# Performance work log

Measured on AMD Instinct MI355X. Metric: run time of the kernel, lower is better.

Reference implementation:

```python
import jax, jax.numpy as jnp
import numpy as np

FIELD_DIMS = [100000] * 39
EMBED_DIM = 16
BATCH = 4096
BETA = 0.01
EPS = 1e-4
OFFSETS = np.concatenate([[0], np.cumsum(FIELD_DIMS)[:-1]]).astype(np.int32)


def setup_inputs() -> dict:
    key = jax.random.key(0)
    k1, k2 = jax.random.split(key)
    x = jax.random.randint(k1, (BATCH, len(FIELD_DIMS)), 0, 100000, dtype=jnp.int32)
    emb_table = jax.random.normal(k2, (sum(FIELD_DIMS), EMBED_DIM), dtype=jnp.float32) * 0.01
    return {"x": x, "emb_table": emb_table}


def reference(x, emb_table):
    # x: [B, F] per-field indices; add per-field offsets then gather -> [B, F, d]
    idx = x + jnp.asarray(OFFSETS)[None, :]
    x_emb = emb_table[idx]
    B, F, _ = x_emb.shape

    # ---- alignment loss: mean over all i<j pairs and fields of ||x_i[f]-x_j[f]||^2.
    # Exact Gram identity: sum_{i<j} ||xi-xj||^2 = B*sum_i ||xi||^2 - ||sum_i xi||^2 (per field).
    sq = jnp.sum(x_emb * x_emb, axis=-1)          # [B, F]
    s = jnp.sum(x_emb, axis=0)                     # [F, d]
    pair_sum = B * jnp.sum(sq) - jnp.sum(s * s)
    n_pairs = B * (B - 1) // 2
    align_loss = pair_sum / (n_pairs * F)

    # ---- uniformity loss: mean of cosine-like similarity over all field pairs per sample.
    frac = jnp.einsum('bfd,bgd->bfg', x_emb, x_emb)   # [B, F, F]
    norms = jnp.sqrt(sq)                               # [B, F]
    denom = norms[:, :, None] * norms[:, None, :] + EPS
    uniform_loss = jnp.mean(frac / denom)

    return (align_loss + uniform_loss) * BETA
```

## Files before the change

kernel.cpp:

```cpp
#include <hip/hip_runtime.h>


#define BATCH   4096
#define NF      39
#define ED      16
#define SPB     8
#define THREADS 256
#define NPAIRS  (NF * (NF + 1) / 2)
#define ROWF    (NF * ED)
#define EPS     1e-4f
#define BETA    0.01

__global__ __launch_bounds__(THREADS) void cl4ctr_main(
    const int* __restrict__ x, const float* __restrict__ emb,
    float* __restrict__ s_glob,
    float* __restrict__ scal)
{
    __shared__ __align__(16) float e[SPB][ROWF];
    __shared__ float norms[SPB][NF + 1];
    __shared__ int   sidx[SPB * NF];
    __shared__ float wred[2][4];

    const int tid = threadIdx.x;
    const int b0  = blockIdx.x * SPB;

    for (int t = tid; t < SPB * NF; t += THREADS)
        sidx[t] = x[b0 * NF + t];
    __syncthreads();

    for (int p = tid; p < SPB * NF * 4; p += THREADS) {
        int si = p / (NF * 4);
        int r  = p - si * (NF * 4);
        int f  = r >> 2, q = r & 3;
        size_t row = (size_t)sidx[si * NF + f] + (size_t)f * 100000u;
        float4 v = *(const float4*)(emb + row * ED + q * 4);
        *(float4*)&e[si][f * ED + q * 4] = v;
    }
    __syncthreads();

    for (int t = tid; t < ROWF; t += THREADS) {
        float a = 0.f;
#pragma unroll
        for (int si = 0; si < SPB; ++si) a += e[si][t];
        atomicAdd(&s_glob[t], a);
    }

    float sq_local = 0.f;
    for (int t = tid; t < SPB * NF; t += THREADS) {
        int si = t / NF, f = t - si * NF;
        const float4* r4 = (const float4*)&e[si][f * ED];
        float4 a = r4[0], b = r4[1], c = r4[2], d = r4[3];
        float sq = a.x*a.x + a.y*a.y + a.z*a.z + a.w*a.w
                 + b.x*b.x + b.y*b.y + b.z*b.z + b.w*b.w
                 + c.x*c.x + c.y*c.y + c.z*c.z + c.w*c.w
                 + d.x*d.x + d.y*d.y + d.z*d.z + d.w*d.w;
        norms[si][f] = sqrtf(sq);
        sq_local += sq;
    }
    __syncthreads();

    float uni = 0.f;
    for (int p = tid; p < SPB * NPAIRS; p += THREADS) {
        int si = p / NPAIRS;
        int k  = p - si * NPAIRS;
        int f = (int)((79.0f - sqrtf((float)(6241 - 8 * k))) * 0.5f);
        if (f > NF - 1) f = NF - 1;
        while (f * (79 - f) / 2 > k) --f;
        while ((f + 1) * (78 - f) / 2 <= k) ++f;
        int g = f + (k - f * (79 - f) / 2);

        const float4* rf = (const float4*)&e[si][f * ED];
        const float4* rg = (const float4*)&e[si][g * ED];
        float4 a0 = rf[0], a1 = rf[1], a2 = rf[2], a3 = rf[3];
        float4 b0 = rg[0], b1 = rg[1], b2 = rg[2], b3 = rg[3];
        float dot = a0.x*b0.x + a0.y*b0.y + a0.z*b0.z + a0.w*b0.w
                  + a1.x*b1.x + a1.y*b1.y + a1.z*b1.z + a1.w*b1.w
                  + a2.x*b2.x + a2.y*b2.y + a2.z*b2.z + a2.w*b2.w
                  + a3.x*b3.x + a3.y*b3.y + a3.z*b3.z + a3.w*b3.w;
        float w = (f == g) ? 1.f : 2.f;
        uni += w * dot / (norms[si][f] * norms[si][g] + EPS);
    }

#pragma unroll
    for (int off = 32; off > 0; off >>= 1) {
        uni      += __shfl_down(uni, off, 64);
        sq_local += __shfl_down(sq_local, off, 64);
    }
    int lane = tid & 63, wv = tid >> 6;
    if (lane == 0) { wred[0][wv] = uni; wred[1][wv] = sq_local; }
    __syncthreads();
    if (tid == 0) {
        atomicAdd(&scal[0], wred[0][0] + wred[0][1] + wred[0][2] + wred[0][3]);
        atomicAdd(&scal[1], wred[1][0] + wred[1][1] + wred[1][2] + wred[1][3]);
    }
}

__global__ __launch_bounds__(256) void cl4ctr_final(
    const float* __restrict__ s_glob, const float* __restrict__ scal,
    float* __restrict__ out)
{
    __shared__ float wred[4];
    float ss = 0.f;
    for (int t = threadIdx.x; t < ROWF; t += 256) {
        float v = s_glob[t];
        ss += v * v;
    }
#pragma unroll
    for (int off = 32; off > 0; off >>= 1)
        ss += __shfl_down(ss, off, 64);
    int lane = threadIdx.x & 63, wv = threadIdx.x >> 6;
    if (lane == 0) wred[wv] = ss;
    __syncthreads();
    if (threadIdx.x == 0) {
        double sstot   = (double)wred[0] + wred[1] + wred[2] + wred[3];
        double uni_sum = (double)scal[0];
        double sq_sum  = (double)scal[1];
        double pair_sum = (double)BATCH * sq_sum - sstot;
        double n_pairs  = (double)BATCH * (BATCH - 1) / 2.0;
        double align_l  = pair_sum / (n_pairs * (double)NF);
        double uniform  = uni_sum / ((double)BATCH * NF * NF);
        out[0] = (float)((align_l + uniform) * BETA);
    }
}

extern "C" void kernel_launch(void* const* d_in, const int* in_sizes, int n_in,
                              void* d_out, int out_size, void* d_ws, size_t ws_size,
                              hipStream_t stream) {
    const int*   x   = (const int*)d_in[0];
    const float* emb = (const float*)d_in[1];
    float* out = (float*)d_out;
    float* ws  = (float*)d_ws;

    hipMemsetAsync(d_ws, 0, 2560, stream);
    cl4ctr_main<<<BATCH / SPB, THREADS, 0, stream>>>(x, emb, ws, ws + ROWF);
    cl4ctr_final<<<1, 256, 0, stream>>>(ws, ws + ROWF, out);
}
```

Before: 323.4 us.

## Pad shared embedding rows and hoist pair index decode out of sample loop

Pads each field row in shared memory from 16 to 20 floats so that float4 reads of different fields spread across LDS banks. The pair loop now decodes each (f,g) pair once and loops over all 8 samples inside it, which removes the per-element division and sqrt-based index recovery. The trade-off is that only 780 of the 256-thread block's work items remain, spread over 4 iterations, so lanes go idle in the last round and register use rises from the unrolled sample loop.

```diff
diff --git a/kernel.cpp b/kernel.cpp
--- a/kernel.cpp
+++ b/kernel.cpp
@@ -4,6 +4,8 @@
 #define BATCH   4096
 #define NF      39
 #define ED      16
+#define FS      20
+#define SS      (FS * NF)
 #define SPB     8
 #define THREADS 256
 #define NPAIRS  (NF * (NF + 1) / 2)
@@ -16,7 +18,7 @@
     float* __restrict__ s_glob,
     float* __restrict__ scal)
 {
-    __shared__ __align__(16) float e[SPB][ROWF];
+    __shared__ __align__(16) float e[SPB * SS];
     __shared__ float norms[SPB][NF + 1];
     __shared__ int   sidx[SPB * NF];
     __shared__ float wred[2][4];
@@ -34,21 +36,22 @@
         int f  = r >> 2, q = r & 3;
         size_t row = (size_t)sidx[si * NF + f] + (size_t)f * 100000u;
         float4 v = *(const float4*)(emb + row * ED + q * 4);
-        *(float4*)&e[si][f * ED + q * 4] = v;
+        *(float4*)&e[si * SS + f * FS + q * 4] = v;
     }
     __syncthreads();
 
     for (int t = tid; t < ROWF; t += THREADS) {
+        int f = t >> 4, d = t & 15;
         float a = 0.f;
 #pragma unroll
-        for (int si = 0; si < SPB; ++si) a += e[si][t];
+        for (int si = 0; si < SPB; ++si) a += e[si * SS + f * FS + d];
         atomicAdd(&s_glob[t], a);
     }
 
     float sq_local = 0.f;
     for (int t = tid; t < SPB * NF; t += THREADS) {
         int si = t / NF, f = t - si * NF;
-        const float4* r4 = (const float4*)&e[si][f * ED];
+        const float4* r4 = (const float4*)&e[si * SS + f * FS];
         float4 a = r4[0], b = r4[1], c = r4[2], d = r4[3];
         float sq = a.x*a.x + a.y*a.y + a.z*a.z + a.w*a.w
                  + b.x*b.x + b.y*b.y + b.z*b.z + b.w*b.w
@@ -60,25 +63,27 @@
     __syncthreads();
 
     float uni = 0.f;
-    for (int p = tid; p < SPB * NPAIRS; p += THREADS) {
-        int si = p / NPAIRS;
-        int k  = p - si * NPAIRS;
-        int f = (int)((79.0f - sqrtf((float)(6241 - 8 * k))) * 0.5f);
+    for (int p = tid; p < NPAIRS; p += THREADS) {
+        int f = (int)((79.0f - sqrtf((float)(6241 - 8 * p))) * 0.5f);
         if (f > NF - 1) f = NF - 1;
-        while (f * (79 - f) / 2 > k) --f;
-        while ((f + 1) * (78 - f) / 2 <= k) ++f;
-        int g = f + (k - f * (79 - f) / 2);
+        while (f * (79 - f) / 2 > p) --f;
+        while ((f + 1) * (78 - f) / 2 <= p) ++f;
+        int g = f + (p - f * (79 - f) / 2);
+        float w = (f == g) ? 1.f : 2.f;
+        int offf = f * FS, offg = g * FS;
 
-        const float4* rf = (const float4*)&e[si][f * ED];
-        const float4* rg = (const float4*)&e[si][g * ED];
-        float4 a0 = rf[0], a1 = rf[1], a2 = rf[2], a3 = rf[3];
-        float4 b0 = rg[0], b1 = rg[1], b2 = rg[2], b3 = rg[3];
-        float dot = a0.x*b0.x + a0.y*b0.y + a0.z*b0.z + a0.w*b0.w
-                  + a1.x*b1.x + a1.y*b1.y + a1.z*b1.z + a1.w*b1.w
-                  + a2.x*b2.x + a2.y*b2.y + a2.z*b2.z + a2.w*b2.w
-                  + a3.x*b3.x + a3.y*b3.y + a3.z*b3.z + a3.w*b3.w;
-        float w = (f == g) ? 1.f : 2.f;
-        uni += w * dot / (norms[si][f] * norms[si][g] + EPS);
+#pragma unroll
+        for (int si = 0; si < SPB; ++si) {
+            const float4* rf = (const float4*)&e[si * SS + offf];
+            const float4* rg = (const float4*)&e[si * SS + offg];
+            float4 a0 = rf[0], a1 = rf[1], a2 = rf[2], a3 = rf[3];
+            float4 b0 = rg[0], b1 = rg[1], b2 = rg[2], b3 = rg[3];
+            float dot = a0.x*b0.x + a0.y*b0.y + a0.z*b0.z + a0.w*b0.w
+                      + a1.x*b1.x + a1.y*b1.y + a1.z*b1.z + a1.w*b1.w
+                      + a2.x*b2.x + a2.y*b2.y + a2.z*b2.z + a2.w*b2.w
+                      + a3.x*b3.x + a3.y*b3.y + a3.z*b3.z + a3.w*b3.w;
+            uni += w * dot / (norms[si][f] * norms[si][g] + EPS);
+        }
     }
 
 #pragma unroll
```

After: 306.4 us. 1.06x faster.
